# Optimization experiments

Measured on AMD Instinct MI355X. Metric: run time of the kernel, lower is better.

## Reference

```python
import jax, jax.numpy as jnp
import numpy as np

K = 20
EPS = 1e-5  # BatchNorm eps; eval mode with running_mean=0, running_var=1


def _lrelu(x):
    return jnp.where(x >= 0, x, 0.2 * x)


def _bn(x, g, b):
    # eval-mode BN (fresh running stats: mean=0, var=1); channel axis = 1
    shape = (1, -1) + (1,) * (x.ndim - 2)
    return x * (g / jnp.sqrt(1.0 + EPS)).reshape(shape) + b.reshape(shape)


def _knn_idx(x, k):
    # x: (B, C, N). Negative squared euclidean distance, top-k = nearest.
    xx = jnp.sum(x * x, axis=1)                      # (B, N)
    inner = jnp.einsum('bcn,bcm->bnm', x, x)         # (B, N, N)
    neg_d = 2.0 * inner - xx[:, :, None] - xx[:, None, :]
    return jax.lax.top_k(neg_d, k)[1]                # (B, N, K)


def _gather(x, idx):
    # x: (B, C, N), idx: (B, N, K) -> (B, C, N, K)
    return jax.vmap(lambda xb, ib: xb[:, ib])(x, idx)


def setup_inputs() -> dict:
    key = jax.random.key(0)
    ks = jax.random.split(key, 32)
    B, N = 8, 2048
    d = {}
    d['x'] = jax.random.normal(ks[0], (B, 3, N), jnp.float32)

    def w(k_, o, i):
        return jax.random.normal(k_, (o, i), jnp.float32) * (1.0 / np.sqrt(i))

    d['W1'] = w(ks[1], 64, 3)
    d['W2'] = w(ks[2], 64, 64)
    d['W3'] = w(ks[3], 128, 64)
    d['W4'] = w(ks[4], 256, 128)
    d['W5'] = w(ks[5], 1024, 512)
    bn_dims = [64, 64, 128, 256, 1024, 512, 256]
    for i, c in enumerate(bn_dims):
        d[f'g{i+1}'] = 1.0 + 0.1 * jax.random.normal(ks[6 + 2 * i], (c,), jnp.float32)
        d[f'b{i+1}'] = 0.1 * jax.random.normal(ks[7 + 2 * i], (c,), jnp.float32)
    d['L1W'] = w(ks[20], 512, 2048)
    d['L2W'] = w(ks[21], 256, 512)
    d['L2b'] = 0.1 * jax.random.normal(ks[22], (256,), jnp.float32)
    d['L3W'] = w(ks[23], 40, 256)
    d['L3b'] = 0.1 * jax.random.normal(ks[24], (40,), jnp.float32)
    return d


def reference(x, W1, W2, W3, W4, W5,
              g1, b1, g2, b2, g3, b3, g4, b4, g5, b5, g6, b6, g7, b7,
              L1W, L2W, L2b, L3W, L3b):
    idx = _knn_idx(x, K)  # shared neighbor indices for all EdgeConv blocks

    h = _lrelu(_bn(jnp.einsum('oc,bcnk->bonk', W1, _gather(x, idx)), g1, b1))
    x1 = h.max(axis=-1)                               # (B, 64, N)
    h = _lrelu(_bn(jnp.einsum('oc,bcnk->bonk', W2, _gather(x1, idx)), g2, b2))
    x2 = h.max(axis=-1)                               # (B, 64, N)
    h = _lrelu(_bn(jnp.einsum('oc,bcnk->bonk', W3, _gather(x2, idx)), g3, b3))
    x3 = h.max(axis=-1)                               # (B, 128, N)
    h = _lrelu(_bn(jnp.einsum('oc,bcnk->bonk', W4, _gather(x3, idx)), g4, b4))
    x4 = h.max(axis=-1)                               # (B, 256, N)

    cat = jnp.concatenate([x1, x2, x3, x4], axis=1)   # (B, 512, N)
    h = _lrelu(_bn(jnp.einsum('oc,bcn->bon', W5, cat), g5, b5))  # (B, 1024, N)

    f = jnp.concatenate([h.max(axis=-1), h.mean(axis=-1)], axis=1)  # (B, 2048)
    f = _lrelu(_bn(f @ L1W.T, g6, b6))
    f = _lrelu(_bn(f @ L2W.T + L2b, g7, b7))          # dropout is identity in eval
    return f @ L3W.T + L3b                            # (B, 40)
```

## Files before the change

### kernel.cpp

```cpp
#include <hip/hip_runtime.h>
#include <math.h>


#define WS_IDX      0
#define WS_Y16      1310720
#define WS_XCAT16   9699328
#define WS_W16      26476544
#define WS_FMAX     27615232
#define WS_FSUM     27648000
#define WS_A1       27680768
#define WS_A2       27697152
#define WS_Y16B     27705344

typedef _Float16 f16x8 __attribute__((ext_vector_type(8)));
typedef float f32x4 __attribute__((ext_vector_type(4)));

struct F3 { float x, y, z; };

__device__ __forceinline__ float lrelu(float v) { return (v >= 0.f) ? v : 0.2f * v; }
__device__ __forceinline__ unsigned sortable_f32(float f) {
  unsigned b = __float_as_uint(f);
  return b ^ (((unsigned)((int)b >> 31)) | 0x80000000u);
}
__device__ __forceinline__ float desort_f32(unsigned u) {
  unsigned b = (u & 0x80000000u) ? (u ^ 0x80000000u) : ~u;
  return __uint_as_float(b);
}

__global__ __launch_bounds__(256) void knn_prep_kernel(
    const float* __restrict__ x, const float* __restrict__ W1,
    const float* __restrict__ g1, const float* __restrict__ b1,
    const float* __restrict__ W2, const float* __restrict__ W3,
    const float* __restrict__ W4, const float* __restrict__ W5,
    _Float16* __restrict__ w16, unsigned* __restrict__ fzero,
    int* __restrict__ idxo, _Float16* __restrict__ xcat) {
  __shared__ F3 pts_s[2048];
  __shared__ unsigned long long cand_s[8][60];
  __shared__ unsigned cnt_s[8];
  __shared__ int sel_s[8][20];
  int tid = threadIdx.x;

  if (blockIdx.x >= 2048) {
    int bid = blockIdx.x - 2048;
#pragma unroll
    for (int t = 0; t < 8; ++t) {
      int i = bid * 2048 + t * 256 + tid;
      if (i < 4096) w16[i] = (_Float16)W2[i];
      else if (i < 12288) w16[i] = (_Float16)W3[i - 4096];
      else if (i < 45056) w16[i] = (_Float16)W4[i - 12288];
      else if (i < 569344) w16[i] = (_Float16)W5[i - 45056];
      else fzero[i - 569344] = 0u;
    }
    return;
  }

  int lwave = tid >> 6, lane = tid & 63;
  int qbase = blockIdx.x * 8;
  int b = qbase >> 11;
  int nbase = qbase & 2047;
  const float* xb = x + b * 6144;
#pragma unroll
  for (int i = 0; i < 8; ++i) {
    int m = tid + i * 256;
    F3 p; p.x = xb[m]; p.y = xb[2048 + m]; p.z = xb[4096 + m];
    pts_s[m] = p;
  }
  if (lane == 0) cnt_s[lwave * 2] = 0, cnt_s[lwave * 2 + 1] = 0;
  __syncthreads();

  F3 q[2];
  float qw[2];
  unsigned keys[2][32];
  unsigned lmax[2] = {0u, 0u};
#pragma unroll
  for (int qi = 0; qi < 2; ++qi) {
    q[qi] = pts_s[nbase + lwave * 2 + qi];
    qw[qi] = q[qi].x * q[qi].x + q[qi].y * q[qi].y + q[qi].z * q[qi].z;
  }
#pragma unroll
  for (int j = 0; j < 32; ++j) {
    F3 p = pts_s[j * 64 + lane];
    float pw = p.x * p.x + p.y * p.y + p.z * p.z;
#pragma unroll
    for (int qi = 0; qi < 2; ++qi) {
      float nd = 2.0f * (q[qi].x * p.x + q[qi].y * p.y + q[qi].z * p.z) -
                 qw[qi] - pw;
      unsigned key = sortable_f32(nd);
      keys[qi][j] = key;
      lmax[qi] = (key > lmax[qi]) ? key : lmax[qi];
    }
  }
  unsigned lo[2] = {0u, 0u}, hi[2] = {0x8001u, 0x8001u};
  for (int it = 0; it < 16; ++it) {
#pragma unroll
    for (int qi = 0; qi < 2; ++qi) {
      unsigned mid = (lo[qi] + hi[qi] + 1) >> 1;
      int cnt = __popcll(__ballot(lmax[qi] >= (mid << 16)));
      if (cnt >= 20) lo[qi] = mid; else hi[qi] = mid;
    }
  }
  unsigned T[2] = {lo[0] << 16, lo[1] << 16};
#pragma unroll
  for (int j = 0; j < 32; ++j) {
    int m = j * 64 + lane;
#pragma unroll
    for (int qi = 0; qi < 2; ++qi) {
      unsigned key = keys[qi][j];
      if (key >= T[qi]) {
        unsigned pos = atomicAdd(&cnt_s[lwave * 2 + qi], 1u);
        if (pos < 60)
          cand_s[lwave * 2 + qi][pos] =
              (((unsigned long long)key) << 32) | (unsigned)(2047 - m);
      }
    }
  }
#pragma unroll
  for (int qi = 0; qi < 2; ++qi) {
    int qq = lwave * 2 + qi;
    int row = qbase + qq;
    int outb = row * 20;
    unsigned C = cnt_s[qq];
    if (C <= 60) {
      unsigned long long v = (lane < (int)C) ? ~cand_s[qq][lane] : ~0ull;
#pragma unroll
      for (int k = 2; k <= 64; k <<= 1) {
#pragma unroll
        for (int jj = k >> 1; jj > 0; jj >>= 1) {
          unsigned long long o = __shfl_xor(v, jj, 64);
          bool lower = (lane & jj) == 0;
          bool up = (lane & k) == 0;
          bool takeMin = (lower == up);
          bool sw = takeMin ? (o < v) : (o > v);
          v = sw ? o : v;
        }
      }
      if (lane < 20) {
        unsigned long long pack = ~v;
        int m = 2047 - (int)(pack & 0xFFFFFFFFu);
        idxo[outb + lane] = m;
        sel_s[qq][lane] = m;
      }
    } else {
      unsigned long long prev = ~0ull;
      for (int r = 0; r < 20; ++r) {
        unsigned long long best = 0ull;
#pragma unroll
        for (int j = 0; j < 32; ++j) {
          int m = j * 64 + lane;
          unsigned long long pk =
              (((unsigned long long)keys[qi][j]) << 32) |
              (unsigned)(2047 - m);
          bool ok = (pk < prev) & (pk > best);
          best = ok ? pk : best;
        }
#pragma unroll
        for (int off = 1; off < 64; off <<= 1) {
          unsigned long long o = __shfl_xor(best, off, 64);
          best = (o > best) ? o : best;
        }
        int m = 2047 - (int)(best & 0xFFFFFFFFu);
        if (lane == 0) { idxo[outb + r] = m; sel_s[qq][r] = m; }
        prev = best;
      }
    }
  }
  float w0 = W1[lane * 3 + 0], w1 = W1[lane * 3 + 1], w2 = W1[lane * 3 + 2];
  float inv = 1.0f / sqrtf(1.0f + 1e-5f);
  float sc = g1[lane] * inv, bi = b1[lane];
#pragma unroll
  for (int qi = 0; qi < 2; ++qi) {
    int qq = lwave * 2 + qi;
    int row = qbase + qq;
    float mx = -3.4e38f, mn = 3.4e38f;
#pragma unroll
    for (int k = 0; k < 20; ++k) {
      F3 p = pts_s[sel_s[qq][k]];
      float v = w0 * p.x + w1 * p.y + w2 * p.z;
      mx = fmaxf(mx, v);
      mn = fminf(mn, v);
    }
    float v = (sc >= 0.0f) ? mx : mn;
    xcat[row * 512 + lane] = (_Float16)lrelu(sc * v + bi);
  }
}

template <int C, int COFF>
__global__ __launch_bounds__(256) void gmax_kernel(const _Float16* __restrict__ y,
                                                   const int* __restrict__ idx,
                                                   const float* __restrict__ g,
                                                   const float* __restrict__ bb,
                                                   _Float16* __restrict__ xcat) {
  constexpr int TP = C / 8;
  int e = blockIdx.x * 256 + threadIdx.x;
  int c8 = e & (TP - 1);
  int pg = e / TP;
  int b = pg >> 11;
  const int* ix = idx + pg * 20;
  int mm[20];
#pragma unroll
  for (int k = 0; k < 20; ++k) mm[k] = ix[k];
  int base = b * 2048 * C + c8 * 8;
  float mx[8], mn[8];
#pragma unroll
  for (int i = 0; i < 8; ++i) { mx[i] = -3.4e38f; mn[i] = 3.4e38f; }
#pragma unroll
  for (int k = 0; k < 20; ++k) {
    f16x8 v = *(const f16x8*)&y[base + mm[k] * C];
#pragma unroll
    for (int i = 0; i < 8; ++i) {
      float f = (float)v[i];
      mx[i] = fmaxf(mx[i], f);
      mn[i] = fminf(mn[i], f);
    }
  }
  float inv = 1.0f / sqrtf(1.0f + 1e-5f);
  f16x8 outv;
#pragma unroll
  for (int i = 0; i < 8; ++i) {
    float s = g[c8 * 8 + i] * inv;
    float v = (s >= 0.0f) ? mx[i] : mn[i];
    outv[i] = (_Float16)lrelu(s * v + bb[c8 * 8 + i]);
  }
  *(f16x8*)&xcat[pg * 512 + COFF + c8 * 8] = outv;
}

template <int CIN, int COUT, int XOFF>
__global__ __launch_bounds__(256) void gemm_mfma(const _Float16* __restrict__ Wh,
                                                 const _Float16* __restrict__ Xc,
                                                 _Float16* __restrict__ Y) {
  constexpr int BN = (COUT < 128) ? COUT : 128;
  constexpr int MT = (BN == 128) ? 4 : 2;
  __shared__ _Float16 Xs[128 * 40];
  __shared__ _Float16 Ws[BN * 40];
  int tid = threadIdx.x;
  int lane = tid & 63, w = tid >> 6;
  int wm = (BN == 128) ? (w & 1) : w;
  int wn = (BN == 128) ? (w >> 1) : 0;
  int col = lane & 15, quad = lane >> 4;
  int pg0 = blockIdx.x * 128;
  int o0 = blockIdx.y * BN;
  int r0 = tid >> 2;
  int c8 = (tid & 3) * 8;
  f32x4 acc[MT][4] = {};
  for (int k0 = 0; k0 < CIN; k0 += 32) {
    f16x8 xa = *(const f16x8*)&Xc[(pg0 + r0) * 512 + XOFF + k0 + c8];
    f16x8 xb2 = *(const f16x8*)&Xc[(pg0 + r0 + 64) * 512 + XOFF + k0 + c8];
    f16x8 wa = *(const f16x8*)&Wh[(o0 + r0) * CIN + k0 + c8];
    f16x8 wb;
    if (BN == 128) wb = *(const f16x8*)&Wh[(o0 + r0 + 64) * CIN + k0 + c8];
    __syncthreads();
    *(f16x8*)&Xs[r0 * 40 + c8] = xa;
    *(f16x8*)&Xs[(r0 + 64) * 40 + c8] = xb2;
    *(f16x8*)&Ws[r0 * 40 + c8] = wa;
    if (BN == 128) *(f16x8*)&Ws[(r0 + 64) * 40 + c8] = wb;
    __syncthreads();
    f16x8 af[MT], bf[4];
#pragma unroll
    for (int t = 0; t < MT; ++t)
      af[t] = *(const f16x8*)&Xs[(wm * (MT * 16) + t * 16 + col) * 40 + quad * 8];
#pragma unroll
    for (int t = 0; t < 4; ++t)
      bf[t] = *(const f16x8*)&Ws[(wn * 64 + t * 16 + col) * 40 + quad * 8];
#pragma unroll
    for (int mt = 0; mt < MT; ++mt)
#pragma unroll
      for (int nt = 0; nt < 4; ++nt)
        acc[mt][nt] = __builtin_amdgcn_mfma_f32_16x16x32_f16(af[mt], bf[nt],
                                                             acc[mt][nt], 0, 0, 0);
  }
#pragma unroll
  for (int mt = 0; mt < MT; ++mt)
#pragma unroll
    for (int nt = 0; nt < 4; ++nt)
#pragma unroll
      for (int r = 0; r < 4; ++r) {
        int p = pg0 + wm * (MT * 16) + mt * 16 + quad * 4 + r;
        int ch = o0 + wn * 64 + nt * 16 + col;
        Y[p * COUT + ch] = (_Float16)acc[mt][nt][r];
      }
}

template <int CIN, int COUT, int XOFF>
__global__ __launch_bounds__(256) void gemm_gather(
    const _Float16* __restrict__ y, const int* __restrict__ idx,
    const float* __restrict__ g, const float* __restrict__ bb,
    const _Float16* __restrict__ Wh, _Float16* __restrict__ xcat,
    _Float16* __restrict__ Yout) {
  constexpr int BN = 128;
  constexpr int MT = 4;
  constexpr int CP = CIN + 8;
  __shared__ _Float16 As[128 * CP];
  __shared__ _Float16 Ws[BN * 40];
  int tid = threadIdx.x;
  int lane = tid & 63, w = tid >> 6;
  int wm = w & 1, wn = w >> 1;
  int col = lane & 15, quad = lane >> 4;
  int pg0 = blockIdx.x * 128;
  int o0 = blockIdx.y * BN;
  const float inv = 1.0f / sqrtf(1.0f + 1e-5f);

  constexpr int TPR = CIN / 8;
#pragma unroll
  for (int t = 0; t < (128 * TPR) / 256; ++t) {
    int task = t * 256 + tid;
    int r = task / TPR;
    int c8 = task % TPR;
    int pg = pg0 + r;
    int b = pg >> 11;
    const int* ix = idx + pg * 20;
    int mm[20];
#pragma unroll
    for (int k = 0; k < 20; ++k) mm[k] = ix[k];
    int base = b * 2048 * CIN + c8 * 8;
    float mx[8], mn[8];
#pragma unroll
    for (int i = 0; i < 8; ++i) { mx[i] = -3.4e38f; mn[i] = 3.4e38f; }
#pragma unroll
    for (int k = 0; k < 20; ++k) {
      f16x8 v = *(const f16x8*)&y[base + mm[k] * CIN];
#pragma unroll
      for (int i = 0; i < 8; ++i) {
        float f = (float)v[i];
        mx[i] = fmaxf(mx[i], f);
        mn[i] = fminf(mn[i], f);
      }
    }
    f16x8 outv;
#pragma unroll
    for (int i = 0; i < 8; ++i) {
      float s = g[c8 * 8 + i] * inv;
      float vv = (s >= 0.0f) ? mx[i] : mn[i];
      outv[i] = (_Float16)lrelu(s * vv + bb[c8 * 8 + i]);
    }
    *(f16x8*)&As[r * CP + c8 * 8] = outv;
    if (blockIdx.y == 0) *(f16x8*)&xcat[pg * 512 + XOFF + c8 * 8] = outv;
  }
  __syncthreads();

  int r0 = tid >> 2;
  int c8b = (tid & 3) * 8;
  f32x4 acc[MT][4] = {};
  for (int k0 = 0; k0 < CIN; k0 += 32) {
    f16x8 wa = *(const f16x8*)&Wh[(o0 + r0) * CIN + k0 + c8b];
    f16x8 wb = *(const f16x8*)&Wh[(o0 + r0 + 64) * CIN + k0 + c8b];
    __syncthreads();
    *(f16x8*)&Ws[r0 * 40 + c8b] = wa;
    *(f16x8*)&Ws[(r0 + 64) * 40 + c8b] = wb;
    __syncthreads();
    f16x8 af[MT], bf[4];
#pragma unroll
    for (int t = 0; t < MT; ++t)
      af[t] = *(const f16x8*)&As[(wm * 64 + t * 16 + col) * CP + k0 + quad * 8];
#pragma unroll
    for (int t = 0; t < 4; ++t)
      bf[t] = *(const f16x8*)&Ws[(wn * 64 + t * 16 + col) * 40 + quad * 8];
#pragma unroll
    for (int mt = 0; mt < MT; ++mt)
#pragma unroll
      for (int nt = 0; nt < 4; ++nt)
        acc[mt][nt] = __builtin_amdgcn_mfma_f32_16x16x32_f16(af[mt], bf[nt],
                                                             acc[mt][nt], 0, 0, 0);
  }
#pragma unroll
  for (int mt = 0; mt < MT; ++mt)
#pragma unroll
    for (int nt = 0; nt < 4; ++nt)
#pragma unroll
      for (int r = 0; r < 4; ++r) {
        int p = pg0 + wm * 64 + mt * 16 + quad * 4 + r;
        int ch = o0 + wn * 64 + nt * 16 + col;
        Yout[p * COUT + ch] = (_Float16)acc[mt][nt][r];
      }
}

typedef const __attribute__((address_space(1))) void* gas1_t;
typedef __attribute__((address_space(3))) void* las3_t;

__device__ __forceinline__ void stage16(const _Float16* g, char* l) {
  __builtin_amdgcn_global_load_lds((gas1_t)g, (las3_t)l, 16, 0, 0);
}

__global__ __launch_bounds__(512, 2) void gemm5_kernel(
    const _Float16* __restrict__ Wh, const _Float16* __restrict__ Xc,
    const float* __restrict__ g5, const float* __restrict__ b5,
    unsigned* __restrict__ fmax, float* __restrict__ fsum) {
  __shared__ __attribute__((aligned(16))) char lds[131072];
  char* ldsc = (char*)lds;
  const int tid = threadIdx.x;
  const int lane = tid & 63, w = tid >> 6;
  const int wm = w & 1, wn = w >> 1;
  const int col = lane & 15, quad = lane >> 4;
  const int pg0 = blockIdx.x * 256;
  const int o0 = blockIdx.y * 256;

  const int so = tid << 4;
  const int sl = so ^ (((so >> 9) & 3) << 5);
  const int srow0 = sl >> 7;
  const int skc0 = (sl & 127) >> 1;

#define STG(srcp, baserow, ktile, regoff, i)                                  \
  stage16((srcp) + ((baserow) + (i) * 64 + srow0) * 512 + (ktile) * 64 + skc0,\
          ldsc + (regoff) + (i) * 8192 + (w << 10))

  const int swc = ((col >> 2) & 3) << 5;
  const int labA = (col * 128 + quad * 16) ^ swc;
  const int labB = ((wn & 1) * 8192 + col * 128 + quad * 16) ^ swc;

#define RDA(m, kk) (*(const f16x8*)(rA + ((labA ^ ((kk) << 6)) + (m) * 2048)))
#define RDB(n, kk) (*(const f16x8*)(rB + ((labB ^ ((kk) << 6)) + (n) * 2048)))

  f32x4 acc[8][4] = {};

  STG(Wh, o0, 0, 32768, 0);       STG(Wh, o0, 0, 32768, 1);
  STG(Wh, o0 + 128, 0, 49152, 0); STG(Wh, o0 + 128, 0, 49152, 1);
  STG(Xc, pg0, 0, 0, 0);          STG(Xc, pg0 + 128, 0, 16384, 0);
  STG(Xc, pg0, 0, 0, 1);          STG(Xc, pg0 + 128, 0, 16384, 1);
  asm volatile("s_waitcnt vmcnt(0)" ::: "memory");
  __builtin_amdgcn_s_barrier();

  for (int t = 0; t < 8; ++t) {
    const int nt = t + 1;
    const char* rA = ldsc + (t & 1) * 65536 + wm * 16384;
    const char* rB = ldsc + (t & 1) * 65536 + 32768 + (wn >> 1) * 16384;
    const int nreg = (nt & 1) * 65536;
    f16x8 bf[4][2];
#pragma unroll
    for (int p = 0; p < 4; ++p) {
      f16x8 a[2][2];
#pragma unroll
      for (int mm = 0; mm < 2; ++mm)
#pragma unroll
        for (int kk = 0; kk < 2; ++kk)
          a[mm][kk] = RDA(2 * p + mm, kk);
      if (p == 0) {
#pragma unroll
        for (int n = 0; n < 4; ++n)
#pragma unroll
          for (int kk = 0; kk < 2; ++kk)
            bf[n][kk] = RDB(n, kk);
      }
      if (t < 7) {
        if (p == 0) { STG(Wh, o0, nt, nreg + 32768, 0);
                      STG(Wh, o0, nt, nreg + 32768, 1); }
        if (p == 1) { STG(Wh, o0 + 128, nt, nreg + 49152, 0);
                      STG(Wh, o0 + 128, nt, nreg + 49152, 1); }
        if (p == 2) { STG(Xc, pg0, nt, nreg + 0, 0);
                      STG(Xc, pg0 + 128, nt, nreg + 16384, 0); }
        if (p == 3) { STG(Xc, pg0, nt, nreg + 0, 1);
                      STG(Xc, pg0 + 128, nt, nreg + 16384, 1); }
      }
      if (p == 1) {
        if (t < 7) { asm volatile("s_waitcnt vmcnt(4)" ::: "memory"); }
        else       { asm volatile("s_waitcnt vmcnt(0)" ::: "memory"); }
      }
      if (p == 3 && t < 7) {
        asm volatile("s_waitcnt vmcnt(2)" ::: "memory");
      }
      __builtin_amdgcn_s_barrier();
      asm volatile("s_waitcnt lgkmcnt(0)" ::: "memory");
      __builtin_amdgcn_sched_barrier(0);
      __builtin_amdgcn_s_setprio(1);
#pragma unroll
      for (int mm = 0; mm < 2; ++mm)
#pragma unroll
        for (int n = 0; n < 4; ++n)
#pragma unroll
          for (int kk = 0; kk < 2; ++kk)
            acc[2 * p + mm][n] = __builtin_amdgcn_mfma_f32_16x16x32_f16(
                a[mm][kk], bf[n][kk], acc[2 * p + mm][n], 0, 0, 0);
      __builtin_amdgcn_s_setprio(0);
      __builtin_amdgcn_s_barrier();
    }
  }
#undef STG
#undef RDA
#undef RDB

  const float inv = 1.0f / sqrtf(1.0f + 1e-5f);
  const int b = pg0 >> 11;
#pragma unroll
  for (int n = 0; n < 4; ++n) {
    int ch = o0 + wn * 64 + n * 16 + col;
    float sc = g5[ch] * inv, bi = b5[ch];
    float mx = -3.4e38f, sm = 0.f;
#pragma unroll
    for (int m = 0; m < 8; ++m)
#pragma unroll
      for (int r = 0; r < 4; ++r) {
        float v = lrelu(acc[m][n][r] * sc + bi);
        mx = fmaxf(mx, v);
        sm += v;
      }
    mx = fmaxf(mx, __shfl_xor(mx, 16, 64));
    sm += __shfl_xor(sm, 16, 64);
    mx = fmaxf(mx, __shfl_xor(mx, 32, 64));
    sm += __shfl_xor(sm, 32, 64);
    if (quad == 0) {
      atomicMax(&fmax[b * 1024 + ch], sortable_f32(mx));
      atomicAdd(&fsum[b * 1024 + ch], sm);
    }
  }
}

__global__ __launch_bounds__(256) void l1_kernel(const unsigned* __restrict__ fmax,
                                                 const float* __restrict__ fsum,
                                                 const float* __restrict__ L1W,
                                                 const float* __restrict__ g6,
                                                 const float* __restrict__ b6,
                                                 float* __restrict__ a1) {
  int gw = (blockIdx.x * 256 + threadIdx.x) >> 6;
  int lane = threadIdx.x & 63;
  int b = gw >> 9, o = gw & 511;
  float s = 0.f;
#pragma unroll
  for (int i = 0; i < 32; ++i) {
    int j = lane + i * 64;
    float fj = (j < 1024) ? desort_f32(fmax[b * 1024 + j])
                          : fsum[b * 1024 + j - 1024] * (1.0f / 2048.0f);
    s += fj * L1W[o * 2048 + j];
  }
#pragma unroll
  for (int off = 1; off < 64; off <<= 1) s += __shfl_xor(s, off, 64);
  if (lane == 0) {
    float scv = g6[o] / sqrtf(1.0f + 1e-5f);
    a1[b * 512 + o] = lrelu(s * scv + b6[o]);
  }
}

__global__ __launch_bounds__(256) void l2_kernel(const float* __restrict__ a1,
                                                 const float* __restrict__ L2W,
                                                 const float* __restrict__ L2b,
                                                 const float* __restrict__ g7,
                                                 const float* __restrict__ b7,
                                                 float* __restrict__ a2) {
  int gw = (blockIdx.x * 256 + threadIdx.x) >> 6;
  int lane = threadIdx.x & 63;
  int b = gw >> 8, o = gw & 255;
  float s = 0.f;
#pragma unroll
  for (int i = 0; i < 8; ++i) {
    int j = lane + i * 64;
    s += a1[b * 512 + j] * L2W[o * 512 + j];
  }
#pragma unroll
  for (int off = 1; off < 64; off <<= 1) s += __shfl_xor(s, off, 64);
  if (lane == 0) {
    float v = s + L2b[o];
    float scv = g7[o] / sqrtf(1.0f + 1e-5f);
    a2[b * 256 + o] = lrelu(v * scv + b7[o]);
  }
}

__global__ __launch_bounds__(256) void l3_kernel(const float* __restrict__ a2,
                                                 const float* __restrict__ L3W,
                                                 const float* __restrict__ L3b,
                                                 float* __restrict__ out) {
  int gw = (blockIdx.x * 256 + threadIdx.x) >> 6;
  int lane = threadIdx.x & 63;
  int b = gw / 40, o = gw % 40;
  float s = 0.f;
#pragma unroll
  for (int i = 0; i < 4; ++i) {
    int j = lane + i * 64;
    s += a2[b * 256 + j] * L3W[o * 256 + j];
  }
#pragma unroll
  for (int off = 1; off < 64; off <<= 1) s += __shfl_xor(s, off, 64);
  if (lane == 0) out[b * 40 + o] = s + L3b[o];
}

extern "C" void kernel_launch(void* const* d_in, const int* in_sizes, int n_in,
                              void* d_out, int out_size, void* d_ws, size_t ws_size,
                              hipStream_t stream) {
  const float* x = (const float*)d_in[0];
  const float* W1 = (const float*)d_in[1];
  const float* W2 = (const float*)d_in[2];
  const float* W3 = (const float*)d_in[3];
  const float* W4 = (const float*)d_in[4];
  const float* W5 = (const float*)d_in[5];
  const float* g1 = (const float*)d_in[6];  const float* b1 = (const float*)d_in[7];
  const float* g2 = (const float*)d_in[8];  const float* b2 = (const float*)d_in[9];
  const float* g3 = (const float*)d_in[10]; const float* b3 = (const float*)d_in[11];
  const float* g4 = (const float*)d_in[12]; const float* b4 = (const float*)d_in[13];
  const float* g5 = (const float*)d_in[14]; const float* b5 = (const float*)d_in[15];
  const float* g6 = (const float*)d_in[16]; const float* b6 = (const float*)d_in[17];
  const float* g7 = (const float*)d_in[18]; const float* b7 = (const float*)d_in[19];
  const float* L1W = (const float*)d_in[20];
  const float* L2W = (const float*)d_in[21];
  const float* L2b = (const float*)d_in[22];
  const float* L3W = (const float*)d_in[23];
  const float* L3b = (const float*)d_in[24];

  char* w = (char*)d_ws;
  int* idxb = (int*)(w + WS_IDX);
  _Float16* y16 = (_Float16*)(w + WS_Y16);
  _Float16* y16b = (_Float16*)(w + WS_Y16B);
  _Float16* xcat16 = (_Float16*)(w + WS_XCAT16);
  _Float16* w16 = (_Float16*)(w + WS_W16);
  unsigned* fmax = (unsigned*)(w + WS_FMAX);
  float* fsum = (float*)(w + WS_FSUM);
  float* a1 = (float*)(w + WS_A1);
  float* a2 = (float*)(w + WS_A2);

  knn_prep_kernel<<<2334, 256, 0, stream>>>(x, W1, g1, b1, W2, W3, W4, W5,
                                            w16, fmax, idxb, xcat16);
  gemm_mfma<64, 64, 0><<<dim3(128, 1), 256, 0, stream>>>(w16, xcat16, y16);
  gemm_gather<64, 128, 64><<<dim3(128, 1), 256, 0, stream>>>(
      y16, idxb, g2, b2, w16 + 4096, xcat16, y16b);
  gemm_gather<128, 256, 128><<<dim3(128, 2), 256, 0, stream>>>(
      y16b, idxb, g3, b3, w16 + 12288, xcat16, y16);
  gmax_kernel<256, 256><<<2048, 256, 0, stream>>>(y16, idxb, g4, b4, xcat16);
  gemm5_kernel<<<dim3(64, 4), 512, 0, stream>>>(w16 + 45056, xcat16, g5, b5, fmax, fsum);
  l1_kernel<<<1024, 256, 0, stream>>>(fmax, fsum, L1W, g6, b6, a1);
  l2_kernel<<<512, 256, 0, stream>>>(a1, L2W, L2b, g7, b7, a2);
  l3_kernel<<<80, 256, 0, stream>>>(a2, L3W, L3b, (float*)d_out);
}
```

Before: 225.5 us.

## Fuse block-3 gather into one 512-thread tile and restructure L1 to reuse weights across batch

```diff
diff --git a/kernel.cpp b/kernel.cpp
--- a/kernel.cpp
+++ b/kernel.cpp
@@ -373,6 +373,96 @@
       }
 }
 
+__global__ __launch_bounds__(512) void gemm_gather256(
+    const _Float16* __restrict__ y, const int* __restrict__ idx,
+    const float* __restrict__ g, const float* __restrict__ bb,
+    const _Float16* __restrict__ Wh, _Float16* __restrict__ xcat,
+    _Float16* __restrict__ Yout) {
+  constexpr int CIN = 128, COUT = 256, XOFF = 128;
+  constexpr int CP = CIN + 8;
+  __shared__ _Float16 As[128 * CP];
+  __shared__ _Float16 Ws[256 * 40];
+  int tid = threadIdx.x;
+  int lane = tid & 63, w = tid >> 6;
+  int wm = w & 1, wn = w >> 1;
+  int col = lane & 15, quad = lane >> 4;
+  int pg0 = blockIdx.x * 128;
+  const float inv = 1.0f / sqrtf(1.0f + 1e-5f);
+
+  constexpr int TPR = CIN / 8;
+#pragma unroll
+  for (int t = 0; t < (128 * TPR) / 512; ++t) {
+    int task = t * 512 + tid;
+    int r = task / TPR;
+    int c8 = task % TPR;
+    int pg = pg0 + r;
+    int b = pg >> 11;
+    const int* ix = idx + pg * 20;
+    int mm[20];
+#pragma unroll
+    for (int k = 0; k < 20; ++k) mm[k] = ix[k];
+    int base = b * 2048 * CIN + c8 * 8;
+    float mx[8], mn[8];
+#pragma unroll
+    for (int i = 0; i < 8; ++i) { mx[i] = -3.4e38f; mn[i] = 3.4e38f; }
+#pragma unroll
+    for (int k = 0; k < 20; ++k) {
+      f16x8 v = *(const f16x8*)&y[base + mm[k] * CIN];
+#pragma unroll
+      for (int i = 0; i < 8; ++i) {
+        float f = (float)v[i];
+        mx[i] = fmaxf(mx[i], f);
+        mn[i] = fminf(mn[i], f);
+      }
+    }
+    f16x8 outv;
+#pragma unroll
+    for (int i = 0; i < 8; ++i) {
+      float s = g[c8 * 8 + i] * inv;
+      float vv = (s >= 0.0f) ? mx[i] : mn[i];
+      outv[i] = (_Float16)lrelu(s * vv + bb[c8 * 8 + i]);
+    }
+    *(f16x8*)&As[r * CP + c8 * 8] = outv;
+    *(f16x8*)&xcat[pg * 512 + XOFF + c8 * 8] = outv;
+  }
+  __syncthreads();
+
+  int r0 = tid >> 1;
+  int c8b = (tid & 1) * 16;
+  f32x4 acc[4][4] = {};
+  for (int k0 = 0; k0 < CIN; k0 += 32) {
+    f16x8 wa = *(const f16x8*)&Wh[r0 * CIN + k0 + c8b];
+    f16x8 wb = *(const f16x8*)&Wh[r0 * CIN + k0 + c8b + 8];
+    __syncthreads();
+    *(f16x8*)&Ws[r0 * 40 + c8b] = wa;
+    *(f16x8*)&Ws[r0 * 40 + c8b + 8] = wb;
+    __syncthreads();
+    f16x8 af[4], bf[4];
+#pragma unroll
+    for (int t = 0; t < 4; ++t)
+      af[t] = *(const f16x8*)&As[(wm * 64 + t * 16 + col) * CP + k0 + quad * 8];
+#pragma unroll
+    for (int t = 0; t < 4; ++t)
+      bf[t] = *(const f16x8*)&Ws[(wn * 64 + t * 16 + col) * 40 + quad * 8];
+#pragma unroll
+    for (int mt = 0; mt < 4; ++mt)
+#pragma unroll
+      for (int nt = 0; nt < 4; ++nt)
+        acc[mt][nt] = __builtin_amdgcn_mfma_f32_16x16x32_f16(af[mt], bf[nt],
+                                                             acc[mt][nt], 0, 0, 0);
+  }
+#pragma unroll
+  for (int mt = 0; mt < 4; ++mt)
+#pragma unroll
+    for (int nt = 0; nt < 4; ++nt)
+#pragma unroll
+      for (int r = 0; r < 4; ++r) {
+        int p = pg0 + wm * 64 + mt * 16 + quad * 4 + r;
+        int ch = wn * 64 + nt * 16 + col;
+        Yout[p * COUT + ch] = (_Float16)acc[mt][nt][r];
+      }
+}
+
 typedef const __attribute__((address_space(1))) void* gas1_t;
 typedef __attribute__((address_space(3))) void* las3_t;
 
@@ -508,22 +598,45 @@
                                                  const float* __restrict__ g6,
                                                  const float* __restrict__ b6,
                                                  float* __restrict__ a1) {
-  int gw = (blockIdx.x * 256 + threadIdx.x) >> 6;
-  int lane = threadIdx.x & 63;
-  int b = gw >> 9, o = gw & 511;
-  float s = 0.f;
-#pragma unroll
-  for (int i = 0; i < 32; ++i) {
-    int j = lane + i * 64;
-    float fj = (j < 1024) ? desort_f32(fmax[b * 1024 + j])
-                          : fsum[b * 1024 + j - 1024] * (1.0f / 2048.0f);
-    s += fj * L1W[o * 2048 + j];
-  }
-#pragma unroll
-  for (int off = 1; off < 64; off <<= 1) s += __shfl_xor(s, off, 64);
-  if (lane == 0) {
+  __shared__ float red[4][8];
+  int o = blockIdx.x;
+  int tid = threadIdx.x, wv = tid >> 6;
+  float4 w0 = *(const float4*)&L1W[o * 2048 + tid * 8];
+  float4 w1 = *(const float4*)&L1W[o * 2048 + tid * 8 + 4];
+  bool isMax = (tid < 128);
+  float sb[8];
+#pragma unroll
+  for (int b = 0; b < 8; ++b) {
+    float s;
+    if (isMax) {
+      uint4 a0 = *(const uint4*)&fmax[b * 1024 + tid * 8];
+      uint4 a1v = *(const uint4*)&fmax[b * 1024 + tid * 8 + 4];
+      s = desort_f32(a0.x) * w0.x + desort_f32(a0.y) * w0.y +
+          desort_f32(a0.z) * w0.z + desort_f32(a0.w) * w0.w +
+          desort_f32(a1v.x) * w1.x + desort_f32(a1v.y) * w1.y +
+          desort_f32(a1v.z) * w1.z + desort_f32(a1v.w) * w1.w;
+    } else {
+      float4 f0 = *(const float4*)&fsum[b * 1024 + tid * 8 - 1024];
+      float4 f1 = *(const float4*)&fsum[b * 1024 + tid * 8 - 1020];
+      s = (f0.x * w0.x + f0.y * w0.y + f0.z * w0.z + f0.w * w0.w +
+           f1.x * w1.x + f1.y * w1.y + f1.z * w1.z + f1.w * w1.w) *
+          (1.0f / 2048.0f);
+    }
+    sb[b] = s;
+  }
+#pragma unroll
+  for (int b = 0; b < 8; ++b)
+#pragma unroll
+    for (int off = 1; off < 64; off <<= 1) sb[b] += __shfl_xor(sb[b], off, 64);
+  if ((tid & 63) == 0) {
+#pragma unroll
+    for (int b = 0; b < 8; ++b) red[wv][b] = sb[b];
+  }
+  __syncthreads();
+  if (tid < 8) {
+    float s = red[0][tid] + red[1][tid] + red[2][tid] + red[3][tid];
     float scv = g6[o] / sqrtf(1.0f + 1e-5f);
-    a1[b * 512 + o] = lrelu(s * scv + b6[o]);
+    a1[tid * 512 + o] = lrelu(s * scv + b6[o]);
   }
 }
 
@@ -607,11 +720,11 @@
   gemm_mfma<64, 64, 0><<<dim3(128, 1), 256, 0, stream>>>(w16, xcat16, y16);
   gemm_gather<64, 128, 64><<<dim3(128, 1), 256, 0, stream>>>(
       y16, idxb, g2, b2, w16 + 4096, xcat16, y16b);
-  gemm_gather<128, 256, 128><<<dim3(128, 2), 256, 0, stream>>>(
+  gemm_gather256<<<dim3(128, 1), 512, 0, stream>>>(
       y16b, idxb, g3, b3, w16 + 12288, xcat16, y16);
   gmax_kernel<256, 256><<<2048, 256, 0, stream>>>(y16, idxb, g4, b4, xcat16);
   gemm5_kernel<<<dim3(64, 4), 512, 0, stream>>>(w16 + 45056, xcat16, g5, b5, fmax, fsum);
-  l1_kernel<<<1024, 256, 0, stream>>>(fmax, fsum, L1W, g6, b6, a1);
+  l1_kernel<<<512, 256, 0, stream>>>(fmax, fsum, L1W, g6, b6, a1);
   l2_kernel<<<512, 256, 0, stream>>>(a1, L2W, L2b, g7, b7, a2);
   l3_kernel<<<80, 256, 0, stream>>>(a2, L3W, L3b, (float*)d_out);
 }
```

Result: faster. 219.9 us (-2.5%).
